# Kernel optimization log

Measured on AMD Instinct MI355X. Metric: run time of the kernel, lower is better.

## Reference

```python
import jax, jax.numpy as jnp
import numpy as np

E, T, D, N_RBF, N_SBF = 262144, 1048576, 128, 6, 42


def setup_inputs() -> dict:
    key = jax.random.key(0)
    ks = jax.random.split(key, 24)
    s = 0.05
    inp = {
        "m_ji": jax.random.normal(ks[0], (E, D), jnp.float32),
        "e_rbf": jax.random.normal(ks[1], (E, N_RBF), jnp.float32),
        "a_sbf": jax.random.normal(ks[2], (T, N_SBF), jnp.float32),
        "nbr_list": jax.random.randint(ks[3], (E, 2), 0, 65536),
        "kj_idx": jax.random.randint(ks[4], (T,), 0, E),
        "ji_idx": jax.random.randint(ks[5], (T,), 0, E),
        # edge branch params
        "We": jax.random.normal(ks[6], (N_RBF, D), jnp.float32) * s,
        "W_e1": jax.random.normal(ks[7], (D, D), jnp.float32) * s,
        "b_e1": jnp.zeros((D,), jnp.float32),
        "W_e2": jax.random.normal(ks[8], (D, D), jnp.float32) * s,
        "b_e2": jnp.zeros((D,), jnp.float32),
        "W_e3": jax.random.normal(ks[9], (D, D), jnp.float32) * s,
        "b_e3": jnp.zeros((D,), jnp.float32),
        "W_e4": jax.random.normal(ks[10], (D, D), jnp.float32) * s,
        # angle branch params
        "Wa": jax.random.normal(ks[11], (N_SBF, D), jnp.float32) * s,
        "W_a1": jax.random.normal(ks[12], (D, D), jnp.float32) * s,
        "b_a1": jnp.zeros((D,), jnp.float32),
        "W_a2": jax.random.normal(ks[13], (D, D), jnp.float32) * s,
        "b_a2": jnp.zeros((D,), jnp.float32),
        "W_a3": jax.random.normal(ks[14], (D, D), jnp.float32) * s,
        "b_a3": jnp.zeros((D,), jnp.float32),
        "W_a4": jax.random.normal(ks[15], (D, D), jnp.float32) * s,
    }
    return inp


def _mlp(x, W1, b1, W2, b2, W3, b3, W4):
    x = jax.nn.silu(x @ W1 + b1)
    x = jax.nn.silu(x @ W2 + b2)
    x = jax.nn.silu(x @ W3 + b3)
    return x @ W4


def reference(m_ji, e_rbf, a_sbf, nbr_list, kj_idx, ji_idx,
              We, W_e1, b_e1, W_e2, b_e2, W_e3, b_e3, W_e4,
              Wa, W_a1, b_a1, W_a2, b_a2, W_a3, b_a3, W_a4):
    # edge branch: project rbf to embed dim, gate by edge messages  [E, D]
    edge_feats = _mlp((e_rbf @ We) * m_ji, W_e1, b_e1, W_e2, b_e2, W_e3, b_e3, W_e4)
    # angle branch: project sbf, gate by triplet-gathered message sum  [T, D]
    angle_gate = m_ji[kj_idx] + m_ji[ji_idx]
    angle_feats = _mlp((a_sbf @ Wa) * angle_gate, W_a1, b_a1, W_a2, b_a2, W_a3, b_a3, W_a4)
    return (edge_feats, angle_feats)
```

## Files before the change

kernel.cpp:

```cpp
#include <hip/hip_runtime.h>
#include <stdint.h>

typedef __attribute__((ext_vector_type(8))) short bf16x8;
typedef __attribute__((ext_vector_type(4))) float f32x4;
typedef __attribute__((ext_vector_type(8))) unsigned short us8;
typedef __attribute__((ext_vector_type(2))) unsigned int u32x2;
typedef __bf16 bf16v2 __attribute__((ext_vector_type(2)));

#define T_CNT 1048576
#define E_CNT 262144

static __device__ __forceinline__ unsigned short f2bf_u(float f) {
  __bf16 h = (__bf16)f;
  return __builtin_bit_cast(unsigned short, h);
}
static __device__ __forceinline__ uint32_t pack2bf(float a, float b) {
  bf16v2 t; t[0] = (__bf16)a; t[1] = (__bf16)b;
  return __builtin_bit_cast(uint32_t, t);
}
static __device__ __forceinline__ float silu_f(float v) {
  float e = __builtin_amdgcn_exp2f(v * -1.44269504088896341f);
  return v * __builtin_amdgcn_rcpf(1.0f + e);
}
static __device__ __forceinline__ bf16x8 frag8(f32x4 a, f32x4 b) {
  union { bf16x8 v; uint32_t u[4]; } r;
  r.u[0] = pack2bf(a[0], a[1]); r.u[1] = pack2bf(a[2], a[3]);
  r.u[2] = pack2bf(b[0], b[1]); r.u[3] = pack2bf(b[2], b[3]);
  return r.v;
}
static __device__ __forceinline__ void gl_lds16(const void* g, void* l) {
  __builtin_amdgcn_global_load_lds(
      (const __attribute__((address_space(1))) void*)g,
      (__attribute__((address_space(3))) void*)l, 16, 0, 0);
}

static __device__ __forceinline__ void mlp4(
    char* __restrict__ xbA, char* __restrict__ xbB,
    const char* __restrict__ wt4,
    const float* __restrict__ b1, const float* __restrict__ b2,
    const float* __restrict__ b3, float* __restrict__ outT,
    int l15, int q, int w, int rs)
{
  const int cb = w * 32;
  #pragma unroll
  for (int L = 0; L < 4; ++L) {
    const char* src = (L & 1) ? xbB : xbA;
    char* dst = (L & 1) ? xbA : xbB;
    bf16x8 wf[2][4];
    #pragma unroll
    for (int ct = 0; ct < 2; ++ct)
      #pragma unroll
      for (int ks = 0; ks < 4; ++ks)
        wf[ct][ks] = *(const bf16x8*)(wt4 + (L << 15) + (((w * 2 + ct) * 4 + ks) << 10) + (l15 | (q << 4)) * 16);
    if (L < 3) {
      const float* bp = (L == 0) ? b1 : (L == 1) ? b2 : b3;
      f32x4 bv0 = *(const f32x4*)(bp + cb + q * 4);
      f32x4 bv1 = *(const f32x4*)(bp + cb + 16 + q * 4);
      #pragma unroll
      for (int rg = 0; rg < 4; ++rg) {
        const int row = rg * 16 + l15;
        f32x4 acc0 = {0.f,0.f,0.f,0.f}, acc1 = {0.f,0.f,0.f,0.f};
        #pragma unroll
        for (int ks = 0; ks < 4; ++ks) {
          bf16x8 xf = *(const bf16x8*)(src + ((row * 256 + ks * 64 + q * 16) ^ rs));
          acc0 = __builtin_amdgcn_mfma_f32_16x16x32_bf16(wf[0][ks], xf, acc0, 0, 0, 0);
          acc1 = __builtin_amdgcn_mfma_f32_16x16x32_bf16(wf[1][ks], xf, acc1, 0, 0, 0);
        }
        uint2 u0, u1;
        u0.x = pack2bf(silu_f(acc0[0] + bv0[0]), silu_f(acc0[1] + bv0[1]));
        u0.y = pack2bf(silu_f(acc0[2] + bv0[2]), silu_f(acc0[3] + bv0[3]));
        u1.x = pack2bf(silu_f(acc1[0] + bv1[0]), silu_f(acc1[1] + bv1[1]));
        u1.y = pack2bf(silu_f(acc1[2] + bv1[2]), silu_f(acc1[3] + bv1[3]));
        *(uint2*)(dst + ((row * 256 + w * 64 + q * 8) ^ rs)) = u0;
        *(uint2*)(dst + ((row * 256 + w * 64 + 32 + q * 8) ^ rs)) = u1;
      }
      __syncthreads();
    } else {
      #pragma unroll
      for (int rg = 0; rg < 4; ++rg) {
        const int row = rg * 16 + l15;
        f32x4 acc0 = {0.f,0.f,0.f,0.f}, acc1 = {0.f,0.f,0.f,0.f};
        #pragma unroll
        for (int ks = 0; ks < 4; ++ks) {
          bf16x8 xf = *(const bf16x8*)(src + ((row * 256 + ks * 64 + q * 16) ^ rs));
          acc0 = __builtin_amdgcn_mfma_f32_16x16x32_bf16(wf[0][ks], xf, acc0, 0, 0, 0);
          acc1 = __builtin_amdgcn_mfma_f32_16x16x32_bf16(wf[1][ks], xf, acc1, 0, 0, 0);
        }
        float* op = outT + (size_t)row * 128 + cb + q * 4;
        __builtin_nontemporal_store(acc0, (f32x4*)(op));
        __builtin_nontemporal_store(acc1, (f32x4*)(op + 16));
      }
    }
  }
}

__global__ __launch_bounds__(256) void angle_proj_kernel(
    const float* __restrict__ m_ji, const float* __restrict__ a_sbf,
    const int* __restrict__ kj, const int* __restrict__ ji,
    const char* __restrict__ waT, char* __restrict__ x0)
{
  const int tid = threadIdx.x, lane = tid & 63, w = tid >> 6;
  const int l15 = lane & 15, q = lane >> 4;
  const int rs = (l15 & 7) << 4;
  const size_t tb = (size_t)blockIdx.x * 64;
  const int rl = w * 16 + l15;
  const size_t grow = tb + rl;

  const int ikj = kj[grow], iji = ji[grow];
  const float* bk = m_ji + (size_t)ikj * 128 + q * 4;
  const float* bj = m_ji + (size_t)iji * 128 + q * 4;

  f32x4 pk[4], pj[4];
  #pragma unroll
  for (int g = 0; g < 4; ++g) {
    pk[g] = *(const f32x4*)(bk + g * 16);
    pj[g] = *(const f32x4*)(bj + g * 16);
  }

  const float* ap = a_sbf + grow * 42;
  f32x4 a0 = *(const f32x4*)(ap + q * 8);
  f32x4 a1 = *(const f32x4*)(ap + q * 8 + 4);
  f32x4 c0 = {0.f,0.f,0.f,0.f}, c1 = {0.f,0.f,0.f,0.f};
  if (q == 0) { c0 = *(const f32x4*)(ap + 32); c1 = *(const f32x4*)(ap + 36); }
  else if (q == 1) { float2 t = *(const float2*)(ap + 40); c0[0] = t.x; c0[1] = t.y; }
  bf16x8 f0 = frag8(a0, a1);
  bf16x8 f1 = frag8(c0, c1);

  char* xrow = x0 + tb * 256 + rl * 256;
  #pragma unroll
  for (int c = 0; c < 8; ++c) {
    bf16x8 wa0 = *(const bf16x8*)(waT + ((c * 2 + 0) << 10) + lane * 16);
    bf16x8 wa1 = *(const bf16x8*)(waT + ((c * 2 + 1) << 10) + lane * 16);
    f32x4 acc = {0.f,0.f,0.f,0.f};
    acc = __builtin_amdgcn_mfma_f32_16x16x32_bf16(wa0, f0, acc, 0, 0, 0);
    acc = __builtin_amdgcn_mfma_f32_16x16x32_bf16(wa1, f1, acc, 0, 0, 0);
    f32x4 g = pk[c & 3] + pj[c & 3];
    if (c < 4) {
      pk[c & 3] = *(const f32x4*)(bk + (c + 4) * 16);
      pj[c & 3] = *(const f32x4*)(bj + (c + 4) * 16);
    }
    u32x2 u;
    u[0] = pack2bf(acc[0] * g[0], acc[1] * g[1]);
    u[1] = pack2bf(acc[2] * g[2], acc[3] * g[3]);
    __builtin_nontemporal_store(u, (u32x2*)(xrow + ((c * 32 + q * 8) ^ rs)));
  }
}

__global__ __launch_bounds__(256) void angle_mlp_kernel(
    const char* __restrict__ x0,
    const float* __restrict__ b1, const float* __restrict__ b2,
    const float* __restrict__ b3,
    const char* __restrict__ wt4, float* __restrict__ out)
{
  __shared__ __align__(16) char xbA[16384];
  __shared__ __align__(16) char xbB[16384];
  const int tid = threadIdx.x, lane = tid & 63, w = tid >> 6;
  const int l15 = lane & 15, q = lane >> 4;
  const int rs = (l15 & 7) << 4;
  const size_t tb = (size_t)blockIdx.x * 64;

  #pragma unroll
  for (int i = 0; i < 4; ++i)
    gl_lds16(x0 + tb * 256 + i * 4096 + tid * 16, xbA + i * 4096 + tid * 16);
  __syncthreads();

  mlp4(xbA, xbB, wt4, b1, b2, b3, out + tb * 128, l15, q, w, rs);
}

__global__ __launch_bounds__(256) void angle_fused_kernel(
    const float* __restrict__ m_ji, const float* __restrict__ a_sbf,
    const int* __restrict__ kj, const int* __restrict__ ji,
    const float* __restrict__ b1, const float* __restrict__ b2,
    const float* __restrict__ b3,
    const char* __restrict__ wt4, const char* __restrict__ waT,
    float* __restrict__ out)
{
  __shared__ __align__(16) char xbA[16384];
  __shared__ __align__(16) char xbB[16384];
  const int tid = threadIdx.x, lane = tid & 63, w = tid >> 6;
  const int l15 = lane & 15, q = lane >> 4;
  const int rs = (l15 & 7) << 4;
  const size_t tb = (size_t)blockIdx.x * 64;
  const int cb = w * 32;

  bf16x8 wa[2][2];
  #pragma unroll
  for (int ct = 0; ct < 2; ++ct)
    #pragma unroll
    for (int ks = 0; ks < 2; ++ks)
      wa[ct][ks] = *(const bf16x8*)(waT + (((w * 2 + ct) * 2 + ks) << 10) + lane * 16);

  int ikj[4], iji[4];
  #pragma unroll
  for (int g = 0; g < 4; ++g) {
    ikj[g] = kj[tb + g * 16 + l15];
    iji[g] = ji[tb + g * 16 + l15];
  }
  f32x4 pk[2][2], pj[2][2];
  auto gissue = [&](int g) {
    const float* bk = m_ji + (size_t)ikj[g] * 128 + cb + q * 4;
    const float* bj = m_ji + (size_t)iji[g] * 128 + cb + q * 4;
    pk[g & 1][0] = *(const f32x4*)(bk);
    pk[g & 1][1] = *(const f32x4*)(bk + 16);
    pj[g & 1][0] = *(const f32x4*)(bj);
    pj[g & 1][1] = *(const f32x4*)(bj + 16);
  };
  gissue(0); gissue(1);

  #pragma unroll
  for (int rg = 0; rg < 4; ++rg) {
    const int row = rg * 16 + l15;
    const float* ap = a_sbf + (tb + row) * 42;
    f32x4 a0 = *(const f32x4*)(ap + q * 8);
    f32x4 a1 = *(const f32x4*)(ap + q * 8 + 4);
    f32x4 c0 = {0.f,0.f,0.f,0.f}, c1 = {0.f,0.f,0.f,0.f};
    if (q == 0) { c0 = *(const f32x4*)(ap + 32); c1 = *(const f32x4*)(ap + 36); }
    else if (q == 1) { float2 t = *(const float2*)(ap + 40); c0[0] = t.x; c0[1] = t.y; }
    bf16x8 f0 = frag8(a0, a1);
    bf16x8 f1 = frag8(c0, c1);
    f32x4 acc0 = {0.f,0.f,0.f,0.f}, acc1 = {0.f,0.f,0.f,0.f};
    acc0 = __builtin_amdgcn_mfma_f32_16x16x32_bf16(wa[0][0], f0, acc0, 0, 0, 0);
    acc0 = __builtin_amdgcn_mfma_f32_16x16x32_bf16(wa[0][1], f1, acc0, 0, 0, 0);
    acc1 = __builtin_amdgcn_mfma_f32_16x16x32_bf16(wa[1][0], f0, acc1, 0, 0, 0);
    acc1 = __builtin_amdgcn_mfma_f32_16x16x32_bf16(wa[1][1], f1, acc1, 0, 0, 0);
    f32x4 g0 = pk[rg & 1][0] + pj[rg & 1][0];
    f32x4 g1 = pk[rg & 1][1] + pj[rg & 1][1];
    if (rg < 2) gissue(rg + 2);
    uint2 u0, u1;
    u0.x = pack2bf(acc0[0] * g0[0], acc0[1] * g0[1]);
    u0.y = pack2bf(acc0[2] * g0[2], acc0[3] * g0[3]);
    u1.x = pack2bf(acc1[0] * g1[0], acc1[1] * g1[1]);
    u1.y = pack2bf(acc1[2] * g1[2], acc1[3] * g1[3]);
    *(uint2*)(xbA + ((row * 256 + w * 64 + q * 8) ^ rs)) = u0;
    *(uint2*)(xbA + ((row * 256 + w * 64 + 32 + q * 8) ^ rs)) = u1;
  }
  __syncthreads();

  mlp4(xbA, xbB, wt4, b1, b2, b3, out + tb * 128, l15, q, w, rs);
}

__global__ __launch_bounds__(256) void edge_kernel(
    const float* __restrict__ m_ji, const float* __restrict__ e_rbf,
    const float* __restrict__ b1, const float* __restrict__ b2,
    const float* __restrict__ b3,
    const char* __restrict__ wt4, const char* __restrict__ weT,
    float* __restrict__ out)
{
  __shared__ __align__(16) char xbA[16384];
  __shared__ __align__(16) char xbB[16384];
  const int tid = threadIdx.x, lane = tid & 63, w = tid >> 6;
  const int l15 = lane & 15, q = lane >> 4;
  const int rs = (l15 & 7) << 4;
  const size_t tb = (size_t)blockIdx.x * 64;
  const int cb = w * 32;

  bf16x8 we[2];
  #pragma unroll
  for (int ct = 0; ct < 2; ++ct)
    we[ct] = *(const bf16x8*)(weT + ((w * 2 + ct) << 10) + lane * 16);

  f32x4 mr[2][2];
  auto missue = [&](int g) {
    const float* bm = m_ji + (tb + g * 16 + l15) * 128 + cb + q * 4;
    mr[g & 1][0] = *(const f32x4*)(bm);
    mr[g & 1][1] = *(const f32x4*)(bm + 16);
  };
  missue(0); missue(1);

  #pragma unroll
  for (int rg = 0; rg < 4; ++rg) {
    const int row = rg * 16 + l15;
    const float* ep = e_rbf + (tb + row) * 6;
    f32x4 a0 = {0.f,0.f,0.f,0.f}, a1 = {0.f,0.f,0.f,0.f};
    if (q == 0) {
      a0 = *(const f32x4*)(ep);
      float2 t = *(const float2*)(ep + 4);
      a1[0] = t.x; a1[1] = t.y;
    }
    bf16x8 ef = frag8(a0, a1);
    f32x4 acc0 = {0.f,0.f,0.f,0.f}, acc1 = {0.f,0.f,0.f,0.f};
    acc0 = __builtin_amdgcn_mfma_f32_16x16x32_bf16(we[0], ef, acc0, 0, 0, 0);
    acc1 = __builtin_amdgcn_mfma_f32_16x16x32_bf16(we[1], ef, acc1, 0, 0, 0);
    f32x4 g0 = mr[rg & 1][0];
    f32x4 g1 = mr[rg & 1][1];
    if (rg < 2) missue(rg + 2);
    uint2 u0, u1;
    u0.x = pack2bf(acc0[0] * g0[0], acc0[1] * g0[1]);
    u0.y = pack2bf(acc0[2] * g0[2], acc0[3] * g0[3]);
    u1.x = pack2bf(acc1[0] * g1[0], acc1[1] * g1[1]);
    u1.y = pack2bf(acc1[2] * g1[2], acc1[3] * g1[3]);
    *(uint2*)(xbA + ((row * 256 + w * 64 + q * 8) ^ rs)) = u0;
    *(uint2*)(xbA + ((row * 256 + w * 64 + 32 + q * 8) ^ rs)) = u1;
  }
  __syncthreads();

  mlp4(xbA, xbB, wt4, b1, b2, b3, out + tb * 128, l15, q, w, rs);
}

__global__ void prep_kernel(
    const float* __restrict__ W0, const float* __restrict__ W1,
    const float* __restrict__ W2, const float* __restrict__ W3,
    const float* __restrict__ W4, const float* __restrict__ W5,
    const float* __restrict__ W6, const float* __restrict__ W7,
    const float* __restrict__ Wa, const float* __restrict__ We,
    char* __restrict__ ws)
{
  const int gid = blockIdx.x * 256 + threadIdx.x;
  const int lane = gid & 63;
  const int l15 = lane & 15, q = lane >> 4;
  if (gid < 16384) {
    const int mat = gid >> 11;
    const int ctks = (gid & 2047) >> 6;
    const int n = (ctks >> 2) * 16 + l15;
    const int k0 = (ctks & 3) * 32 + q * 8;
    const float* W;
    switch (mat) {
      case 0: W = W0; break; case 1: W = W1; break;
      case 2: W = W2; break; case 3: W = W3; break;
      case 4: W = W4; break; case 5: W = W5; break;
      case 6: W = W6; break; default: W = W7; break;
    }
    us8 v;
    #pragma unroll
    for (int j = 0; j < 8; ++j) v[j] = f2bf_u(W[(size_t)(k0 + j) * 128 + n]);
    *(us8*)(ws + mat * 32768 + ctks * 1024 + lane * 16) = v;
  } else if (gid < 17408) {
    const int g = gid - 16384;
    const int ctks = g >> 6;
    const int n = (ctks >> 1) * 16 + l15;
    const int k0 = (ctks & 1) * 32 + q * 8;
    us8 v;
    #pragma unroll
    for (int j = 0; j < 8; ++j) {
      const int k = k0 + j;
      v[j] = (k < 42) ? f2bf_u(Wa[(size_t)k * 128 + n]) : (unsigned short)0;
    }
    *(us8*)(ws + 262144 + ctks * 1024 + lane * 16) = v;
  } else if (gid < 17920) {
    const int g = gid - 17408;
    const int ct = g >> 6;
    const int n = ct * 16 + l15;
    const int k0 = q * 8;
    us8 v;
    #pragma unroll
    for (int j = 0; j < 8; ++j) {
      const int k = k0 + j;
      v[j] = (k < 6) ? f2bf_u(We[(size_t)k * 128 + n]) : (unsigned short)0;
    }
    *(us8*)(ws + 278528 + ct * 1024 + lane * 16) = v;
  }
}

extern "C" void kernel_launch(void* const* d_in, const int* in_sizes, int n_in,
                              void* d_out, int out_size, void* d_ws, size_t ws_size,
                              hipStream_t stream) {
  (void)in_sizes; (void)n_in; (void)out_size;
  const float* m_ji  = (const float*)d_in[0];
  const float* e_rbf = (const float*)d_in[1];
  const float* a_sbf = (const float*)d_in[2];
  const int*   kj    = (const int*)d_in[4];
  const int*   ji    = (const int*)d_in[5];
  const float* We    = (const float*)d_in[6];
  const float* We1   = (const float*)d_in[7];
  const float* be1   = (const float*)d_in[8];
  const float* We2   = (const float*)d_in[9];
  const float* be2   = (const float*)d_in[10];
  const float* We3   = (const float*)d_in[11];
  const float* be3   = (const float*)d_in[12];
  const float* We4   = (const float*)d_in[13];
  const float* Wa    = (const float*)d_in[14];
  const float* Wa1   = (const float*)d_in[15];
  const float* ba1   = (const float*)d_in[16];
  const float* Wa2   = (const float*)d_in[17];
  const float* ba2   = (const float*)d_in[18];
  const float* Wa3   = (const float*)d_in[19];
  const float* ba3   = (const float*)d_in[20];
  const float* Wa4   = (const float*)d_in[21];
  char* ws = (char*)d_ws;
  float* out = (float*)d_out;
  float* out_a = out + (size_t)E_CNT * 128;

  prep_kernel<<<70, 256, 0, stream>>>(
      We1, We2, We3, We4, Wa1, Wa2, Wa3, Wa4, Wa, We, ws);
  edge_kernel<<<E_CNT / 64, 256, 0, stream>>>(
      m_ji, e_rbf, be1, be2, be3, ws, ws + 278528, out);

  const size_t x0_off = 1u << 20;
  const size_t need = x0_off + (size_t)T_CNT * 256;
  if (ws_size >= need) {
    char* x0 = ws + x0_off;
    angle_proj_kernel<<<T_CNT / 64, 256, 0, stream>>>(
        m_ji, a_sbf, kj, ji, ws + 262144, x0);
    angle_mlp_kernel<<<T_CNT / 64, 256, 0, stream>>>(
        x0, ba1, ba2, ba3, ws + 131072, out_a);
  } else {
    angle_fused_kernel<<<T_CNT / 64, 256, 0, stream>>>(
        m_ji, a_sbf, kj, ji, ba1, ba2, ba3, ws + 131072, ws + 262144, out_a);
  }
}
```

Measured before the change: 596.2 us.

## Restructure angle MLP so each wave owns 32 rows with wave-private LDS

The angle MLP kernel now runs 128 threads per block, and each wave processes its own 32 rows end to end. It loads the input fragments straight from global memory into registers instead of staging them through LDS, then ping-pongs activations through a wave-private 8 KB LDS slice. This removes block-wide barriers and the shared double buffer, and cuts LDS per block. The cost is that each wave now loads all 128 output columns of weights for every layer. The proj kernel's row addressing is rewritten to match.

```diff
diff --git a/kernel.cpp b/kernel.cpp
--- a/kernel.cpp
+++ b/kernel.cpp
@@ -27,11 +27,6 @@
   r.u[0] = pack2bf(a[0], a[1]); r.u[1] = pack2bf(a[2], a[3]);
   r.u[2] = pack2bf(b[0], b[1]); r.u[3] = pack2bf(b[2], b[3]);
   return r.v;
-}
-static __device__ __forceinline__ void gl_lds16(const void* g, void* l) {
-  __builtin_amdgcn_global_load_lds(
-      (const __attribute__((address_space(1))) void*)g,
-      (__attribute__((address_space(3))) void*)l, 16, 0, 0);
 }
 
 static __device__ __forceinline__ void mlp4(
@@ -126,7 +121,7 @@
   bf16x8 f0 = frag8(a0, a1);
   bf16x8 f1 = frag8(c0, c1);
 
-  char* xrow = x0 + tb * 256 + rl * 256;
+  char* xrow = x0 + grow * 256;
   #pragma unroll
   for (int c = 0; c < 8; ++c) {
     bf16x8 wa0 = *(const bf16x8*)(waT + ((c * 2 + 0) << 10) + lane * 16);
@@ -146,25 +141,81 @@
   }
 }
 
-__global__ __launch_bounds__(256) void angle_mlp_kernel(
+__global__ __launch_bounds__(128) void angle_mlp_kernel(
     const char* __restrict__ x0,
     const float* __restrict__ b1, const float* __restrict__ b2,
     const float* __restrict__ b3,
     const char* __restrict__ wt4, float* __restrict__ out)
 {
-  __shared__ __align__(16) char xbA[16384];
-  __shared__ __align__(16) char xbB[16384];
+  __shared__ __align__(16) char sl[16384];
   const int tid = threadIdx.x, lane = tid & 63, w = tid >> 6;
   const int l15 = lane & 15, q = lane >> 4;
   const int rs = (l15 & 7) << 4;
-  const size_t tb = (size_t)blockIdx.x * 64;
-
-  #pragma unroll
-  for (int i = 0; i < 4; ++i)
-    gl_lds16(x0 + tb * 256 + i * 4096 + tid * 16, xbA + i * 4096 + tid * 16);
-  __syncthreads();
-
-  mlp4(xbA, xbB, wt4, b1, b2, b3, out + tb * 128, l15, q, w, rs);
+  char* slice = sl + w * 8192;
+  const size_t grow0 = ((size_t)blockIdx.x * 2 + w) * 32;
+  const int lane16 = lane * 16;
+
+  bf16x8 xf[2][4];
+  #pragma unroll
+  for (int rg = 0; rg < 2; ++rg)
+    #pragma unroll
+    for (int ks = 0; ks < 4; ++ks)
+      xf[rg][ks] = *(const bf16x8*)(
+          x0 + (grow0 + rg * 16 + l15) * 256 + ((ks * 64 + q * 16) ^ rs));
+
+  #pragma unroll
+  for (int L = 0; L < 4; ++L) {
+    const char* wbase = wt4 + (L << 15);
+    if (L > 0) {
+      #pragma unroll
+      for (int rg = 0; rg < 2; ++rg)
+        #pragma unroll
+        for (int ks = 0; ks < 4; ++ks)
+          xf[rg][ks] = *(const bf16x8*)(
+              slice + (((rg * 16 + l15) * 256 + ks * 64 + q * 16) ^ rs));
+    }
+    if (L < 3) {
+      const float* bp = (L == 0) ? b1 : (L == 1) ? b2 : b3;
+      #pragma unroll
+      for (int ct = 0; ct < 8; ++ct) {
+        bf16x8 wf0 = *(const bf16x8*)(wbase + ((ct * 4 + 0) << 10) + lane16);
+        bf16x8 wf1 = *(const bf16x8*)(wbase + ((ct * 4 + 1) << 10) + lane16);
+        bf16x8 wf2 = *(const bf16x8*)(wbase + ((ct * 4 + 2) << 10) + lane16);
+        bf16x8 wf3 = *(const bf16x8*)(wbase + ((ct * 4 + 3) << 10) + lane16);
+        f32x4 bv = *(const f32x4*)(bp + ct * 16 + q * 4);
+        #pragma unroll
+        for (int rg = 0; rg < 2; ++rg) {
+          f32x4 acc = {0.f,0.f,0.f,0.f};
+          acc = __builtin_amdgcn_mfma_f32_16x16x32_bf16(wf0, xf[rg][0], acc, 0, 0, 0);
+          acc = __builtin_amdgcn_mfma_f32_16x16x32_bf16(wf1, xf[rg][1], acc, 0, 0, 0);
+          acc = __builtin_amdgcn_mfma_f32_16x16x32_bf16(wf2, xf[rg][2], acc, 0, 0, 0);
+          acc = __builtin_amdgcn_mfma_f32_16x16x32_bf16(wf3, xf[rg][3], acc, 0, 0, 0);
+          uint2 u;
+          u.x = pack2bf(silu_f(acc[0] + bv[0]), silu_f(acc[1] + bv[1]));
+          u.y = pack2bf(silu_f(acc[2] + bv[2]), silu_f(acc[3] + bv[3]));
+          *(uint2*)(slice + (((rg * 16 + l15) * 256 + ct * 32 + q * 8) ^ rs)) = u;
+        }
+      }
+    } else {
+      #pragma unroll
+      for (int ct = 0; ct < 8; ++ct) {
+        bf16x8 wf0 = *(const bf16x8*)(wbase + ((ct * 4 + 0) << 10) + lane16);
+        bf16x8 wf1 = *(const bf16x8*)(wbase + ((ct * 4 + 1) << 10) + lane16);
+        bf16x8 wf2 = *(const bf16x8*)(wbase + ((ct * 4 + 2) << 10) + lane16);
+        bf16x8 wf3 = *(const bf16x8*)(wbase + ((ct * 4 + 3) << 10) + lane16);
+        #pragma unroll
+        for (int rg = 0; rg < 2; ++rg) {
+          f32x4 acc = {0.f,0.f,0.f,0.f};
+          acc = __builtin_amdgcn_mfma_f32_16x16x32_bf16(wf0, xf[rg][0], acc, 0, 0, 0);
+          acc = __builtin_amdgcn_mfma_f32_16x16x32_bf16(wf1, xf[rg][1], acc, 0, 0, 0);
+          acc = __builtin_amdgcn_mfma_f32_16x16x32_bf16(wf2, xf[rg][2], acc, 0, 0, 0);
+          acc = __builtin_amdgcn_mfma_f32_16x16x32_bf16(wf3, xf[rg][3], acc, 0, 0, 0);
+          __builtin_nontemporal_store(acc,
+              (f32x4*)(out + (grow0 + rg * 16 + l15) * 128 + ct * 16 + q * 4));
+        }
+      }
+    }
+  }
 }
 
 __global__ __launch_bounds__(256) void angle_fused_kernel(
@@ -391,7 +442,7 @@
     char* x0 = ws + x0_off;
     angle_proj_kernel<<<T_CNT / 64, 256, 0, stream>>>(
         m_ji, a_sbf, kj, ji, ws + 262144, x0);
-    angle_mlp_kernel<<<T_CNT / 64, 256, 0, stream>>>(
+    angle_mlp_kernel<<<T_CNT / 64, 128, 0, stream>>>(
         x0, ba1, ba2, ba3, ws + 131072, out_a);
   } else {
     angle_fused_kernel<<<T_CNT / 64, 256, 0, stream>>>(
```

Result: slower. 723.0 us (+21.3%).

## Drop split angle path, use fused angle kernel with 32-row tiles

Applied to the files above, without the earlier changes.

Removes the two-kernel angle path that staged the gated projection through a bf16 workspace buffer and always runs the fused projection+MLP kernel instead. Both edge and angle kernels now process 32 rows per block instead of 64, halving LDS buffers and doubling grid size. This removes a round trip through global memory for the intermediate activations but halves the reuse of weight fragments loaded per block and drops the software-pipelined gather prefetch.

```diff
diff --git a/kernel.cpp b/kernel.cpp
--- a/kernel.cpp
+++ b/kernel.cpp
@@ -4,7 +4,6 @@
 typedef __attribute__((ext_vector_type(8))) short bf16x8;
 typedef __attribute__((ext_vector_type(4))) float f32x4;
 typedef __attribute__((ext_vector_type(8))) unsigned short us8;
-typedef __attribute__((ext_vector_type(2))) unsigned int u32x2;
 typedef __bf16 bf16v2 __attribute__((ext_vector_type(2)));
 
 #define T_CNT 1048576
@@ -27,11 +26,6 @@
   r.u[0] = pack2bf(a[0], a[1]); r.u[1] = pack2bf(a[2], a[3]);
   r.u[2] = pack2bf(b[0], b[1]); r.u[3] = pack2bf(b[2], b[3]);
   return r.v;
-}
-static __device__ __forceinline__ void gl_lds16(const void* g, void* l) {
-  __builtin_amdgcn_global_load_lds(
-      (const __attribute__((address_space(1))) void*)g,
-      (__attribute__((address_space(3))) void*)l, 16, 0, 0);
 }
 
 static __device__ __forceinline__ void mlp4(
@@ -57,7 +51,7 @@
       f32x4 bv0 = *(const f32x4*)(bp + cb + q * 4);
       f32x4 bv1 = *(const f32x4*)(bp + cb + 16 + q * 4);
       #pragma unroll
-      for (int rg = 0; rg < 4; ++rg) {
+      for (int rg = 0; rg < 2; ++rg) {
         const int row = rg * 16 + l15;
         f32x4 acc0 = {0.f,0.f,0.f,0.f}, acc1 = {0.f,0.f,0.f,0.f};
         #pragma unroll
@@ -77,7 +71,7 @@
       __syncthreads();
     } else {
       #pragma unroll
-      for (int rg = 0; rg < 4; ++rg) {
+      for (int rg = 0; rg < 2; ++rg) {
         const int row = rg * 16 + l15;
         f32x4 acc0 = {0.f,0.f,0.f,0.f}, acc1 = {0.f,0.f,0.f,0.f};
         #pragma unroll
@@ -94,80 +88,7 @@
   }
 }
 
-__global__ __launch_bounds__(256) void angle_proj_kernel(
-    const float* __restrict__ m_ji, const float* __restrict__ a_sbf,
-    const int* __restrict__ kj, const int* __restrict__ ji,
-    const char* __restrict__ waT, char* __restrict__ x0)
-{
-  const int tid = threadIdx.x, lane = tid & 63, w = tid >> 6;
-  const int l15 = lane & 15, q = lane >> 4;
-  const int rs = (l15 & 7) << 4;
-  const size_t tb = (size_t)blockIdx.x * 64;
-  const int rl = w * 16 + l15;
-  const size_t grow = tb + rl;
-
-  const int ikj = kj[grow], iji = ji[grow];
-  const float* bk = m_ji + (size_t)ikj * 128 + q * 4;
-  const float* bj = m_ji + (size_t)iji * 128 + q * 4;
-
-  f32x4 pk[4], pj[4];
-  #pragma unroll
-  for (int g = 0; g < 4; ++g) {
-    pk[g] = *(const f32x4*)(bk + g * 16);
-    pj[g] = *(const f32x4*)(bj + g * 16);
-  }
-
-  const float* ap = a_sbf + grow * 42;
-  f32x4 a0 = *(const f32x4*)(ap + q * 8);
-  f32x4 a1 = *(const f32x4*)(ap + q * 8 + 4);
-  f32x4 c0 = {0.f,0.f,0.f,0.f}, c1 = {0.f,0.f,0.f,0.f};
-  if (q == 0) { c0 = *(const f32x4*)(ap + 32); c1 = *(const f32x4*)(ap + 36); }
-  else if (q == 1) { float2 t = *(const float2*)(ap + 40); c0[0] = t.x; c0[1] = t.y; }
-  bf16x8 f0 = frag8(a0, a1);
-  bf16x8 f1 = frag8(c0, c1);
-
-  char* xrow = x0 + tb * 256 + rl * 256;
-  #pragma unroll
-  for (int c = 0; c < 8; ++c) {
-    bf16x8 wa0 = *(const bf16x8*)(waT + ((c * 2 + 0) << 10) + lane * 16);
-    bf16x8 wa1 = *(const bf16x8*)(waT + ((c * 2 + 1) << 10) + lane * 16);
-    f32x4 acc = {0.f,0.f,0.f,0.f};
-    acc = __builtin_amdgcn_mfma_f32_16x16x32_bf16(wa0, f0, acc, 0, 0, 0);
-    acc = __builtin_amdgcn_mfma_f32_16x16x32_bf16(wa1, f1, acc, 0, 0, 0);
-    f32x4 g = pk[c & 3] + pj[c & 3];
-    if (c < 4) {
-      pk[c & 3] = *(const f32x4*)(bk + (c + 4) * 16);
-      pj[c & 3] = *(const f32x4*)(bj + (c + 4) * 16);
-    }
-    u32x2 u;
-    u[0] = pack2bf(acc[0] * g[0], acc[1] * g[1]);
-    u[1] = pack2bf(acc[2] * g[2], acc[3] * g[3]);
-    __builtin_nontemporal_store(u, (u32x2*)(xrow + ((c * 32 + q * 8) ^ rs)));
-  }
-}
-
-__global__ __launch_bounds__(256) void angle_mlp_kernel(
-    const char* __restrict__ x0,
-    const float* __restrict__ b1, const float* __restrict__ b2,
-    const float* __restrict__ b3,
-    const char* __restrict__ wt4, float* __restrict__ out)
-{
-  __shared__ __align__(16) char xbA[16384];
-  __shared__ __align__(16) char xbB[16384];
-  const int tid = threadIdx.x, lane = tid & 63, w = tid >> 6;
-  const int l15 = lane & 15, q = lane >> 4;
-  const int rs = (l15 & 7) << 4;
-  const size_t tb = (size_t)blockIdx.x * 64;
-
-  #pragma unroll
-  for (int i = 0; i < 4; ++i)
-    gl_lds16(x0 + tb * 256 + i * 4096 + tid * 16, xbA + i * 4096 + tid * 16);
-  __syncthreads();
-
-  mlp4(xbA, xbB, wt4, b1, b2, b3, out + tb * 128, l15, q, w, rs);
-}
-
-__global__ __launch_bounds__(256) void angle_fused_kernel(
+__global__ __launch_bounds__(256) void angle_kernel(
     const float* __restrict__ m_ji, const float* __restrict__ a_sbf,
     const int* __restrict__ kj, const int* __restrict__ ji,
     const float* __restrict__ b1, const float* __restrict__ b2,
@@ -175,12 +96,12 @@
     const char* __restrict__ wt4, const char* __restrict__ waT,
     float* __restrict__ out)
 {
-  __shared__ __align__(16) char xbA[16384];
-  __shared__ __align__(16) char xbB[16384];
+  __shared__ __align__(16) char xbA[8192];
+  __shared__ __align__(16) char xbB[8192];
   const int tid = threadIdx.x, lane = tid & 63, w = tid >> 6;
   const int l15 = lane & 15, q = lane >> 4;
   const int rs = (l15 & 7) << 4;
-  const size_t tb = (size_t)blockIdx.x * 64;
+  const size_t tb = (size_t)blockIdx.x * 32;
   const int cb = w * 32;
 
   bf16x8 wa[2][2];
@@ -190,25 +111,25 @@
     for (int ks = 0; ks < 2; ++ks)
       wa[ct][ks] = *(const bf16x8*)(waT + (((w * 2 + ct) * 2 + ks) << 10) + lane * 16);
 
-  int ikj[4], iji[4];
-  #pragma unroll
-  for (int g = 0; g < 4; ++g) {
+  int ikj[2], iji[2];
+  #pragma unroll
+  for (int g = 0; g < 2; ++g) {
     ikj[g] = kj[tb + g * 16 + l15];
     iji[g] = ji[tb + g * 16 + l15];
   }
   f32x4 pk[2][2], pj[2][2];
-  auto gissue = [&](int g) {
+  #pragma unroll
+  for (int g = 0; g < 2; ++g) {
     const float* bk = m_ji + (size_t)ikj[g] * 128 + cb + q * 4;
     const float* bj = m_ji + (size_t)iji[g] * 128 + cb + q * 4;
-    pk[g & 1][0] = *(const f32x4*)(bk);
-    pk[g & 1][1] = *(const f32x4*)(bk + 16);
-    pj[g & 1][0] = *(const f32x4*)(bj);
-    pj[g & 1][1] = *(const f32x4*)(bj + 16);
-  };
-  gissue(0); gissue(1);
-
-  #pragma unroll
-  for (int rg = 0; rg < 4; ++rg) {
+    pk[g][0] = *(const f32x4*)(bk);
+    pk[g][1] = *(const f32x4*)(bk + 16);
+    pj[g][0] = *(const f32x4*)(bj);
+    pj[g][1] = *(const f32x4*)(bj + 16);
+  }
+
+  #pragma unroll
+  for (int rg = 0; rg < 2; ++rg) {
     const int row = rg * 16 + l15;
     const float* ap = a_sbf + (tb + row) * 42;
     f32x4 a0 = *(const f32x4*)(ap + q * 8);
@@ -223,9 +144,8 @@
     acc0 = __builtin_amdgcn_mfma_f32_16x16x32_bf16(wa[0][1], f1, acc0, 0, 0, 0);
     acc1 = __builtin_amdgcn_mfma_f32_16x16x32_bf16(wa[1][0], f0, acc1, 0, 0, 0);
     acc1 = __builtin_amdgcn_mfma_f32_16x16x32_bf16(wa[1][1], f1, acc1, 0, 0, 0);
-    f32x4 g0 = pk[rg & 1][0] + pj[rg & 1][0];
-    f32x4 g1 = pk[rg & 1][1] + pj[rg & 1][1];
-    if (rg < 2) gissue(rg + 2);
+    f32x4 g0 = pk[rg][0] + pj[rg][0];
+    f32x4 g1 = pk[rg][1] + pj[rg][1];
     uint2 u0, u1;
     u0.x = pack2bf(acc0[0] * g0[0], acc0[1] * g0[1]);
     u0.y = pack2bf(acc0[2] * g0[2], acc0[3] * g0[3]);
@@ -246,12 +166,12 @@
     const char* __restrict__ wt4, const char* __restrict__ weT,
     float* __restrict__ out)
 {
-  __shared__ __align__(16) char xbA[16384];
-  __shared__ __align__(16) char xbB[16384];
+  __shared__ __align__(16) char xbA[8192];
+  __shared__ __align__(16) char xbB[8192];
   const int tid = threadIdx.x, lane = tid & 63, w = tid >> 6;
   const int l15 = lane & 15, q = lane >> 4;
   const int rs = (l15 & 7) << 4;
-  const size_t tb = (size_t)blockIdx.x * 64;
+  const size_t tb = (size_t)blockIdx.x * 32;
   const int cb = w * 32;
 
   bf16x8 we[2];
@@ -260,15 +180,15 @@
     we[ct] = *(const bf16x8*)(weT + ((w * 2 + ct) << 10) + lane * 16);
 
   f32x4 mr[2][2];
-  auto missue = [&](int g) {
+  #pragma unroll
+  for (int g = 0; g < 2; ++g) {
     const float* bm = m_ji + (tb + g * 16 + l15) * 128 + cb + q * 4;
-    mr[g & 1][0] = *(const f32x4*)(bm);
-    mr[g & 1][1] = *(const f32x4*)(bm + 16);
-  };
-  missue(0); missue(1);
-
-  #pragma unroll
-  for (int rg = 0; rg < 4; ++rg) {
+    mr[g][0] = *(const f32x4*)(bm);
+    mr[g][1] = *(const f32x4*)(bm + 16);
+  }
+
+  #pragma unroll
+  for (int rg = 0; rg < 2; ++rg) {
     const int row = rg * 16 + l15;
     const float* ep = e_rbf + (tb + row) * 6;
     f32x4 a0 = {0.f,0.f,0.f,0.f}, a1 = {0.f,0.f,0.f,0.f};
@@ -281,9 +201,8 @@
     f32x4 acc0 = {0.f,0.f,0.f,0.f}, acc1 = {0.f,0.f,0.f,0.f};
     acc0 = __builtin_amdgcn_mfma_f32_16x16x32_bf16(we[0], ef, acc0, 0, 0, 0);
     acc1 = __builtin_amdgcn_mfma_f32_16x16x32_bf16(we[1], ef, acc1, 0, 0, 0);
-    f32x4 g0 = mr[rg & 1][0];
-    f32x4 g1 = mr[rg & 1][1];
-    if (rg < 2) missue(rg + 2);
+    f32x4 g0 = mr[rg][0];
+    f32x4 g1 = mr[rg][1];
     uint2 u0, u1;
     u0.x = pack2bf(acc0[0] * g0[0], acc0[1] * g0[1]);
     u0.y = pack2bf(acc0[2] * g0[2], acc0[3] * g0[3]);
@@ -354,7 +273,7 @@
 extern "C" void kernel_launch(void* const* d_in, const int* in_sizes, int n_in,
                               void* d_out, int out_size, void* d_ws, size_t ws_size,
                               hipStream_t stream) {
-  (void)in_sizes; (void)n_in; (void)out_size;
+  (void)in_sizes; (void)n_in; (void)out_size; (void)ws_size;
   const float* m_ji  = (const float*)d_in[0];
   const float* e_rbf = (const float*)d_in[1];
   const float* a_sbf = (const float*)d_in[2];
@@ -382,19 +301,8 @@
 
   prep_kernel<<<70, 256, 0, stream>>>(
       We1, We2, We3, We4, Wa1, Wa2, Wa3, Wa4, Wa, We, ws);
-  edge_kernel<<<E_CNT / 64, 256, 0, stream>>>(
+  edge_kernel<<<E_CNT / 32, 256, 0, stream>>>(
       m_ji, e_rbf, be1, be2, be3, ws, ws + 278528, out);
-
-  const size_t x0_off = 1u << 20;
-  const size_t need = x0_off + (size_t)T_CNT * 256;
-  if (ws_size >= need) {
-    char* x0 = ws + x0_off;
-    angle_proj_kernel<<<T_CNT / 64, 256, 0, stream>>>(
-        m_ji, a_sbf, kj, ji, ws + 262144, x0);
-    angle_mlp_kernel<<<T_CNT / 64, 256, 0, stream>>>(
-        x0, ba1, ba2, ba3, ws + 131072, out_a);
-  } else {
-    angle_fused_kernel<<<T_CNT / 64, 256, 0, stream>>>(
-        m_ji, a_sbf, kj, ji, ba1, ba2, ba3, ws + 131072, ws + 262144, out_a);
-  }
-}
+  angle_kernel<<<T_CNT / 32, 256, 0, stream>>>(
+      m_ji, a_sbf, kj, ji, ba1, ba2, ba3, ws + 131072, ws + 262144, out_a);
+}
```

Measured after the change: 602.2 us. Within noise of the previous version (+1.0%).
